# Optimization experiments

Measured on AMD Instinct MI355X. Metric: run time of the kernel, lower is better.

Reference implementation:

```python
import jax, jax.numpy as jnp
import numpy as np

N_NODES = 100000
K = 10
ALPHA = 0.1


def _gcn_norm(ei, n):
    # add self loops (PyG APPNP default: add_self_loops=True, gcn_norm)
    loops = jnp.arange(n, dtype=ei.dtype)
    src = jnp.concatenate([ei[0], loops])
    dst = jnp.concatenate([ei[1], loops])
    ones = jnp.ones(src.shape[0], dtype=jnp.float32)
    deg = jax.ops.segment_sum(ones, dst, num_segments=n)
    dinv = jnp.where(deg > 0, jax.lax.rsqrt(deg), 0.0)
    norm = dinv[src] * dinv[dst]  # [E+N]
    return src, dst, norm


def reference(x, ei, W1, b1, W2, b2):
    n = x.shape[0]
    # MLP encoder (dropout is identity in eval mode)
    h = jax.nn.relu(x @ W1 + b1)
    h = h @ W2 + b2  # [N, out_c]
    src, dst, norm = _gcn_norm(ei, n)
    h0 = h
    for _ in range(K):
        msg = norm[:, None] * h[src]                      # gather [E+N, out_c]
        agg = jax.ops.segment_sum(msg, dst, num_segments=n)  # scatter-add
        h = (1.0 - ALPHA) * agg + ALPHA * h0
    return h


def setup_inputs() -> dict:
    key = jax.random.key(0)
    k1, k2, k3, k4 = jax.random.split(key, 4)
    in_c, hidden, out_c = 512, 256, 64
    E = 3200000
    x = jax.random.normal(k1, (N_NODES, in_c), dtype=jnp.float32)
    ei = jax.random.randint(k2, (2, E), 0, N_NODES, dtype=jnp.int64)
    s1 = 1.0 / np.sqrt(in_c)
    s2 = 1.0 / np.sqrt(hidden)
    W1 = jax.random.uniform(k3, (in_c, hidden), jnp.float32, -s1, s1)
    b1 = jnp.zeros((hidden,), jnp.float32)
    W2 = jax.random.uniform(k4, (hidden, out_c), jnp.float32, -s2, s2)
    b2 = jnp.zeros((out_c,), jnp.float32)
    return {"x": x, "ei": ei, "W1": W1, "b1": b1, "W2": W2, "b2": b2}
```

## Files before the change

kernel.cpp:

```cpp
#include <hip/hip_runtime.h>


typedef unsigned short u16;
typedef unsigned int   u32;
typedef __bf16    bfx8  __attribute__((ext_vector_type(8)));
typedef _Float16  h16x8 __attribute__((ext_vector_type(8)));
typedef float     f32x4 __attribute__((ext_vector_type(4)));

#define CAP 4096
#define EPB 16384
#define NBMAX 1792

__device__ __forceinline__ u16 f2bf(float f) {
    u32 u = __float_as_uint(f);
    u += 0x7fffu + ((u >> 16) & 1u);
    return (u16)(u >> 16);
}


__global__ __launch_bounds__(256) void binscat_kernel(
        const int* __restrict__ src, const int* __restrict__ dst,
        int* __restrict__ gcur, u32* __restrict__ binned, int E, int NB) {
    __shared__ int cnt[NBMAX];
    int tid = threadIdx.x;
#pragma unroll
    for (int j = 0; j < NBMAX / 256; ++j) cnt[tid + j * 256] = 0;
    __syncthreads();
    int e0 = blockIdx.x * EPB;
    for (int r = 0; r < EPB / 256; ++r) {
        int i = e0 + r * 256 + tid;
        if (i < E) atomicAdd(&cnt[dst[i] >> 6], 1);
    }
    __syncthreads();
    for (int j = 0; j < NBMAX / 256; ++j) {
        int b = tid + j * 256;
        if (b < NB) {
            int c = cnt[b];
            cnt[b] = (c > 0) ? atomicAdd(&gcur[b], c) : 0;
        }
    }
    __syncthreads();
    for (int r = 0; r < EPB / 256; ++r) {
        int i = e0 + r * 256 + tid;
        if (i < E) {
            int d = dst[i];
            int s = src[i];
            int bb = d >> 6;
            int p = atomicAdd(&cnt[bb], 1);
            if (p < CAP) binned[(size_t)bb * CAP + p] = ((u32)(d & 63) << 17) | (u32)s;
        }
    }
}


__global__ __launch_bounds__(256) void bucket_scan_kernel(
        const int* __restrict__ gcur, int* __restrict__ bbase,
        int* __restrict__ rp, int N, int NB) {
    __shared__ int tsum[256];
    int tid = threadIdx.x;
    int loc[7];
    int run = 0;
#pragma unroll
    for (int j = 0; j < 7; ++j) {
        int b = tid * 7 + j;
        int v = 0;
        if (b < NB) { v = gcur[b]; if (v > CAP) v = CAP; }
        loc[j] = run;
        run += v;
    }
    tsum[tid] = run;
    __syncthreads();
    for (int off = 1; off < 256; off <<= 1) {
        int t = (tid >= off) ? tsum[tid - off] : 0;
        __syncthreads();
        tsum[tid] += t;
        __syncthreads();
    }
    int texcl = tsum[tid] - run;
#pragma unroll
    for (int j = 0; j < 7; ++j) {
        int b = tid * 7 + j;
        if (b < NB) bbase[b] = texcl + loc[j];
    }
    if (tid == 255) rp[N] = tsum[255];
}


__global__ __launch_bounds__(256) void buildcsr_kernel(
        const u32* __restrict__ binned, const int* __restrict__ gcur,
        const int* __restrict__ bbase, int* __restrict__ rp,
        float* __restrict__ dinv, int* __restrict__ csr, int N) {
    __shared__ u32 eb[CAP];
    __shared__ int lcsr[CAP];
    __shared__ int ncnt[64];
    __shared__ int lcur[64];
    int b = blockIdx.x;
    int tid = threadIdx.x;
    int cnt = gcur[b]; if (cnt > CAP) cnt = CAP;
    int base = bbase[b];
    if (tid < 64) ncnt[tid] = 0;
    __syncthreads();
    for (int idx = tid; idx < cnt; idx += 256) {
        u32 v = binned[(size_t)b * CAP + idx];
        eb[idx] = v;
        atomicAdd(&ncnt[v >> 17], 1);
    }
    __syncthreads();
    if (tid < 64) {
        int c = ncnt[tid];
        int s = c;
#pragma unroll
        for (int off = 1; off < 64; off <<= 1) {
            int t = __shfl_up(s, off);
            if (tid >= off) s += t;
        }
        int excl = s - c;
        lcur[tid] = excl;
        int node = b * 64 + tid;
        if (node < N) {
            rp[node] = base + excl;
            dinv[node] = rsqrtf(1.0f + (float)c);
        }
    }
    __syncthreads();
    for (int idx = tid; idx < cnt; idx += 256) {
        u32 v = eb[idx];
        int p = atomicAdd(&lcur[v >> 17], 1);
        lcsr[p] = (int)(v & 0x1FFFFu);
    }
    __syncthreads();
    for (int idx = tid; idx < cnt; idx += 256)
        csr[base + idx] = lcsr[idx];
}


__global__ void prepw1_kernel(const float* __restrict__ W1, u16* __restrict__ W1t) {
    int id = blockIdx.x * 256 + threadIdx.x;
    int k = id >> 8, n = id & 255;
    W1t[n * 512 + k] = f2bf(W1[id]);
}

__global__ void prepw2_kernel(const float* __restrict__ W2, u16* __restrict__ W2t) {
    int id = blockIdx.x * 256 + threadIdx.x;
    int k = id >> 6, n = id & 63;
    W2t[n * 256 + k] = f2bf(W2[id]);
}


__global__ __launch_bounds__(256) void mlp_kernel(
        const float* __restrict__ x, const u16* __restrict__ W1t,
        const float* __restrict__ b1, const u16* __restrict__ W2t,
        const float* __restrict__ b2, const float* __restrict__ dinv,
        float* __restrict__ h0, _Float16* __restrict__ hA, int N) {
    __shared__ char lds[65536];
    u16* xs  = (u16*)lds;
    u16* w1s = (u16*)(lds + 5120);
    u16* h1s = (u16*)lds;
    u16* w2s = (u16*)(lds + 32768);

    const int tid  = threadIdx.x;
    const int wave = tid >> 6;
    const int lane = tid & 63;
    const int lq   = lane >> 4;
    const int lr   = lane & 15;
    const int blockRow = blockIdx.x * 64;

    f32x4 acc[4][4];
#pragma unroll
    for (int a = 0; a < 4; ++a)
#pragma unroll
        for (int b = 0; b < 4; ++b) acc[a][b] = (f32x4){0.f, 0.f, 0.f, 0.f};

    for (int kk = 0; kk < 512; kk += 32) {
        __syncthreads();
        {
            int r = tid >> 2, c = (tid & 3) << 3;
            int gr = blockRow + r;
            float v[8];
            if (gr < N) {
                const float* p = x + (size_t)gr * 512 + kk + c;
                float4 u0 = *(const float4*)p;
                float4 u1 = *(const float4*)(p + 4);
                v[0]=u0.x; v[1]=u0.y; v[2]=u0.z; v[3]=u0.w;
                v[4]=u1.x; v[5]=u1.y; v[6]=u1.z; v[7]=u1.w;
            } else {
#pragma unroll
                for (int j = 0; j < 8; ++j) v[j] = 0.f;
            }
            u32 pk[4];
#pragma unroll
            for (int j = 0; j < 4; ++j)
                pk[j] = (u32)f2bf(v[2*j]) | ((u32)f2bf(v[2*j+1]) << 16);
            uint4 st = make_uint4(pk[0], pk[1], pk[2], pk[3]);
            *(uint4*)&xs[r * 40 + c] = st;
        }
        {
            const uint4* p = (const uint4*)(W1t + (size_t)tid * 512 + kk);
            uint4* q = (uint4*)&w1s[tid * 40];
            q[0] = p[0]; q[1] = p[1]; q[2] = p[2]; q[3] = p[3];
        }
        __syncthreads();
        bfx8 fa[4], fb[4];
#pragma unroll
        for (int mt = 0; mt < 4; ++mt)
            fa[mt] = *(bfx8*)&xs[(mt * 16 + lr) * 40 + lq * 8];
#pragma unroll
        for (int nt = 0; nt < 4; ++nt)
            fb[nt] = *(bfx8*)&w1s[(wave * 64 + nt * 16 + lr) * 40 + lq * 8];
#pragma unroll
        for (int mt = 0; mt < 4; ++mt)
#pragma unroll
            for (int nt = 0; nt < 4; ++nt)
                acc[mt][nt] = __builtin_amdgcn_mfma_f32_16x16x32_bf16(
                    fa[mt], fb[nt], acc[mt][nt], 0, 0, 0);
    }
    __syncthreads();

#pragma unroll
    for (int nt = 0; nt < 4; ++nt) {
        int col = wave * 64 + nt * 16 + lr;
        float bb = b1[col];
#pragma unroll
        for (int mt = 0; mt < 4; ++mt)
#pragma unroll
            for (int r = 0; r < 4; ++r) {
                int row = mt * 16 + lq * 4 + r;
                float v = acc[mt][nt][r] + bb;
                v = v > 0.f ? v : 0.f;
                h1s[row * 256 + col] = f2bf(v);
            }
    }
    {
        int nn = tid >> 2, seg = (tid & 3) * 64;
        const uint4* p = (const uint4*)(W2t + nn * 256 + seg);
        uint4* q = (uint4*)&w2s[nn * 256 + seg];
#pragma unroll
        for (int j = 0; j < 8; ++j) q[j] = p[j];
    }
    __syncthreads();

    f32x4 acc2[4];
#pragma unroll
    for (int a = 0; a < 4; ++a) acc2[a] = (f32x4){0.f, 0.f, 0.f, 0.f};
    for (int kk = 0; kk < 256; kk += 32) {
        bfx8 a = *(bfx8*)&h1s[(wave * 16 + lr) * 256 + kk + lq * 8];
#pragma unroll
        for (int nt = 0; nt < 4; ++nt) {
            bfx8 b = *(bfx8*)&w2s[(nt * 16 + lr) * 256 + kk + lq * 8];
            acc2[nt] = __builtin_amdgcn_mfma_f32_16x16x32_bf16(a, b, acc2[nt], 0, 0, 0);
        }
    }
#pragma unroll
    for (int nt = 0; nt < 4; ++nt) {
        int col = nt * 16 + lr;
        float bb = b2[col];
#pragma unroll
        for (int r = 0; r < 4; ++r) {
            int row = wave * 16 + lq * 4 + r;
            int gr = blockRow + row;
            if (gr < N) {
                float v = acc2[nt][r] + bb;
                size_t idx = (size_t)gr * 64 + col;
                h0[idx] = v;
                hA[idx] = (_Float16)(v * dinv[gr]);
            }
        }
    }
}


template <typename OUTT>
__global__ __launch_bounds__(256) void prop_kernel(
        const _Float16* __restrict__ hs, const float* __restrict__ h0,
        const float* __restrict__ dinv, const int* __restrict__ rp,
        const int* __restrict__ csr, OUTT* __restrict__ hout, int N) {
    int t = blockIdx.x * 256 + threadIdx.x;
    int i = t >> 3;
    int l = t & 7;
    if (i >= N) return;
    int beg = rp[i], end = rp[i + 1];
    const _Float16* hb = hs + l * 8;
    h16x8 self = *(const h16x8*)(hb + (size_t)i * 64);
    float a[8];
#pragma unroll
    for (int j = 0; j < 8; ++j) a[j] = (float)self[j];
    int e = beg;
    for (; e + 1 < end; e += 2) {
        int s0 = csr[e], s1 = csr[e + 1];
        h16x8 g0 = *(const h16x8*)(hb + (size_t)s0 * 64);
        h16x8 g1 = *(const h16x8*)(hb + (size_t)s1 * 64);
#pragma unroll
        for (int j = 0; j < 8; ++j) a[j] += (float)g0[j];
#pragma unroll
        for (int j = 0; j < 8; ++j) a[j] += (float)g1[j];
    }
    if (e < end) {
        int s0 = csr[e];
        h16x8 g0 = *(const h16x8*)(hb + (size_t)s0 * 64);
#pragma unroll
        for (int j = 0; j < 8; ++j) a[j] += (float)g0[j];
    }
    float dv = dinv[i];
    float c1 = 0.9f * dv;
    const float* h0p = h0 + (size_t)i * 64 + l * 8;
    float o[8];
#pragma unroll
    for (int j = 0; j < 8; ++j) o[j] = fmaf(c1, a[j], 0.1f * h0p[j]);
    if constexpr (sizeof(OUTT) == 2) {
        h16x8 ov;
#pragma unroll
        for (int j = 0; j < 8; ++j) ov[j] = (_Float16)(dv * o[j]);
        *(h16x8*)(hout + (size_t)i * 64 + l * 8) = ov;
    } else {
        float4* q = (float4*)(hout + (size_t)i * 64 + l * 8);
        q[0] = make_float4(o[0], o[1], o[2], o[3]);
        q[1] = make_float4(o[4], o[5], o[6], o[7]);
    }
}


extern "C" void kernel_launch(void* const* d_in, const int* in_sizes, int n_in,
                              void* d_out, int out_size, void* d_ws, size_t ws_size,
                              hipStream_t stream) {
    const float* x  = (const float*)d_in[0];
    const int*   ei = (const int*)d_in[1];
    const float* W1 = (const float*)d_in[2];
    const float* b1 = (const float*)d_in[3];
    const float* W2 = (const float*)d_in[4];
    const float* b2 = (const float*)d_in[5];
    const int N = in_sizes[0] / 512;
    const int E = in_sizes[1] / 2;
    const int NB = (N + 63) / 64;
    const int* src = ei;
    const int* dst = ei + E;

    char* w = (char*)d_ws;
    size_t off = 0;
    auto alloc = [&](size_t bytes) -> char* {
        char* p = w + off;
        off = (off + bytes + 1023) & ~(size_t)1023;
        return p;
    };
    int*      gcur  = (int*)alloc((size_t)NB * 4);
    int*      bbase = (int*)alloc((size_t)NB * 4);
    int*      rp    = (int*)alloc(((size_t)N + 1) * 4);
    float*    dinv  = (float*)alloc((size_t)N * 4);
    int*      csr   = (int*)alloc((size_t)E * 4);
    u32*      binned= (u32*)alloc((size_t)NB * CAP * 4);
    u16*      W1t   = (u16*)alloc(512 * 256 * 2);
    u16*      W2t   = (u16*)alloc(256 * 64 * 2);
    float*    h0    = (float*)alloc((size_t)N * 64 * 4);
    _Float16* hA    = (_Float16*)alloc((size_t)N * 64 * 2);
    _Float16* hB    = (_Float16*)alloc((size_t)N * 64 * 2);

    hipMemsetAsync(gcur, 0, (size_t)NB * 4, stream);
    binscat_kernel<<<(E + EPB - 1) / EPB, 256, 0, stream>>>(src, dst, gcur, binned, E, NB);
    bucket_scan_kernel<<<1, 256, 0, stream>>>(gcur, bbase, rp, N, NB);
    buildcsr_kernel<<<NB, 256, 0, stream>>>(binned, gcur, bbase, rp, dinv, csr, N);
    prepw1_kernel<<<512, 256, 0, stream>>>(W1, W1t);
    prepw2_kernel<<<64, 256, 0, stream>>>(W2, W2t);
    mlp_kernel<<<(N + 63) / 64, 256, 0, stream>>>(x, W1t, b1, W2t, b2, dinv, h0, hA, N);

    const _Float16* pin = hA;
    int grid = (N * 8 + 255) / 256;
    for (int it = 0; it < 9; ++it) {
        _Float16* pout = (it & 1) ? hA : hB;
        prop_kernel<_Float16><<<grid, 256, 0, stream>>>(pin, h0, dinv, rp, csr, pout, N);
        pin = pout;
    }
    prop_kernel<float><<<grid, 256, 0, stream>>>(pin, h0, dinv, rp, csr, (float*)d_out, N);
}
```

Measured before the change: 1.087 ms.

## Pre-pack MLP weights into MFMA fragment order and double-buffer x tiles

Result: faster. 1.056 ms (-2.8%).

```diff
diff --git a/kernel.cpp b/kernel.cpp
--- a/kernel.cpp
+++ b/kernel.cpp
@@ -134,29 +134,50 @@
 }
 
 
-__global__ void prepw1_kernel(const float* __restrict__ W1, u16* __restrict__ W1t) {
-    int id = blockIdx.x * 256 + threadIdx.x;
-    int k = id >> 8, n = id & 255;
-    W1t[n * 512 + k] = f2bf(W1[id]);
-}
-
-__global__ void prepw2_kernel(const float* __restrict__ W2, u16* __restrict__ W2t) {
-    int id = blockIdx.x * 256 + threadIdx.x;
-    int k = id >> 6, n = id & 63;
-    W2t[n * 256 + k] = f2bf(W2[id]);
+__global__ void prepw1_kernel(const float* __restrict__ W1, u16* __restrict__ W1f) {
+    int f = blockIdx.x * 256 + threadIdx.x;
+    int lane = f & 63;
+    int nt = (f >> 6) & 3;
+    int w  = (f >> 8) & 3;
+    int t  = f >> 10;
+    int col = w * 64 + nt * 16 + (lane & 15);
+    int k0  = t * 32 + ((lane >> 4) << 3);
+    u32 pk[4];
+#pragma unroll
+    for (int j = 0; j < 4; ++j) {
+        u16 lo = f2bf(W1[(size_t)(k0 + 2 * j) * 256 + col]);
+        u16 hi = f2bf(W1[(size_t)(k0 + 2 * j + 1) * 256 + col]);
+        pk[j] = (u32)lo | ((u32)hi << 16);
+    }
+    *(uint4*)&W1f[(size_t)f * 8] = make_uint4(pk[0], pk[1], pk[2], pk[3]);
+}
+
+__global__ void prepw2_kernel(const float* __restrict__ W2, u16* __restrict__ W2f) {
+    int f = blockIdx.x * 256 + threadIdx.x;
+    int lane = f & 63;
+    int nt = (f >> 6) & 3;
+    int t  = f >> 8;
+    int col = nt * 16 + (lane & 15);
+    int k0  = t * 32 + ((lane >> 4) << 3);
+    u32 pk[4];
+#pragma unroll
+    for (int j = 0; j < 4; ++j) {
+        u16 lo = f2bf(W2[(size_t)(k0 + 2 * j) * 64 + col]);
+        u16 hi = f2bf(W2[(size_t)(k0 + 2 * j + 1) * 64 + col]);
+        pk[j] = (u32)lo | ((u32)hi << 16);
+    }
+    *(uint4*)&W2f[(size_t)f * 8] = make_uint4(pk[0], pk[1], pk[2], pk[3]);
 }
 
 
 __global__ __launch_bounds__(256) void mlp_kernel(
-        const float* __restrict__ x, const u16* __restrict__ W1t,
-        const float* __restrict__ b1, const u16* __restrict__ W2t,
+        const float* __restrict__ x, const u16* __restrict__ W1f,
+        const float* __restrict__ b1, const u16* __restrict__ W2f,
         const float* __restrict__ b2, const float* __restrict__ dinv,
         float* __restrict__ h0, _Float16* __restrict__ hA, int N) {
-    __shared__ char lds[65536];
+    __shared__ char lds[32768];
     u16* xs  = (u16*)lds;
-    u16* w1s = (u16*)(lds + 5120);
     u16* h1s = (u16*)lds;
-    u16* w2s = (u16*)(lds + 32768);
 
     const int tid  = threadIdx.x;
     const int wave = tid >> 6;
@@ -165,54 +186,73 @@
     const int lr   = lane & 15;
     const int blockRow = blockIdx.x * 64;
 
+    const int sr = tid >> 2;
+    const int sc = (tid & 3) << 3;
+    const int gr = blockRow + sr;
+    const bool haveRow = (gr < N);
+    const float* xp = x + (size_t)(haveRow ? gr : 0) * 512 + sc;
+
     f32x4 acc[4][4];
 #pragma unroll
     for (int a = 0; a < 4; ++a)
 #pragma unroll
         for (int b = 0; b < 4; ++b) acc[a][b] = (f32x4){0.f, 0.f, 0.f, 0.f};
 
-    for (int kk = 0; kk < 512; kk += 32) {
+    {
+        float v[8];
+#pragma unroll
+        for (int j = 0; j < 8; ++j) v[j] = 0.f;
+        if (haveRow) {
+            float4 u0 = *(const float4*)(xp);
+            float4 u1 = *(const float4*)(xp + 4);
+            v[0]=u0.x; v[1]=u0.y; v[2]=u0.z; v[3]=u0.w;
+            v[4]=u1.x; v[5]=u1.y; v[6]=u1.z; v[7]=u1.w;
+        }
+        u32 pk[4];
+#pragma unroll
+        for (int j = 0; j < 4; ++j)
+            pk[j] = (u32)f2bf(v[2*j]) | ((u32)f2bf(v[2*j+1]) << 16);
+        *(uint4*)&xs[sr * 40 + sc] = make_uint4(pk[0], pk[1], pk[2], pk[3]);
+    }
+
+    const bfx8* w1q = (const bfx8*)W1f;
+
+    for (int t = 0; t < 16; ++t) {
+        bfx8 fb0 = w1q[(t * 16 + wave * 4 + 0) * 64 + lane];
+        bfx8 fb1 = w1q[(t * 16 + wave * 4 + 1) * 64 + lane];
+        bfx8 fb2 = w1q[(t * 16 + wave * 4 + 2) * 64 + lane];
+        bfx8 fb3 = w1q[(t * 16 + wave * 4 + 3) * 64 + lane];
+        float v[8];
+#pragma unroll
+        for (int j = 0; j < 8; ++j) v[j] = 0.f;
+        if (t < 15 && haveRow) {
+            const float* p = xp + (t + 1) * 32;
+            float4 u0 = *(const float4*)(p);
+            float4 u1 = *(const float4*)(p + 4);
+            v[0]=u0.x; v[1]=u0.y; v[2]=u0.z; v[3]=u0.w;
+            v[4]=u1.x; v[5]=u1.y; v[6]=u1.z; v[7]=u1.w;
+        }
         __syncthreads();
-        {
-            int r = tid >> 2, c = (tid & 3) << 3;
-            int gr = blockRow + r;
-            float v[8];
-            if (gr < N) {
-                const float* p = x + (size_t)gr * 512 + kk + c;
-                float4 u0 = *(const float4*)p;
-                float4 u1 = *(const float4*)(p + 4);
-                v[0]=u0.x; v[1]=u0.y; v[2]=u0.z; v[3]=u0.w;
-                v[4]=u1.x; v[5]=u1.y; v[6]=u1.z; v[7]=u1.w;
-            } else {
-#pragma unroll
-                for (int j = 0; j < 8; ++j) v[j] = 0.f;
-            }
+        const u16* cur = xs + (t & 1) * 2560;
+        bfx8 fa[4];
+#pragma unroll
+        for (int mt = 0; mt < 4; ++mt)
+            fa[mt] = *(const bfx8*)&cur[(mt * 16 + lr) * 40 + lq * 8];
+#pragma unroll
+        for (int mt = 0; mt < 4; ++mt) {
+            acc[mt][0] = __builtin_amdgcn_mfma_f32_16x16x32_bf16(fa[mt], fb0, acc[mt][0], 0, 0, 0);
+            acc[mt][1] = __builtin_amdgcn_mfma_f32_16x16x32_bf16(fa[mt], fb1, acc[mt][1], 0, 0, 0);
+            acc[mt][2] = __builtin_amdgcn_mfma_f32_16x16x32_bf16(fa[mt], fb2, acc[mt][2], 0, 0, 0);
+            acc[mt][3] = __builtin_amdgcn_mfma_f32_16x16x32_bf16(fa[mt], fb3, acc[mt][3], 0, 0, 0);
+        }
+        if (t < 15) {
+            u16* nxt = xs + ((t + 1) & 1) * 2560;
             u32 pk[4];
 #pragma unroll
             for (int j = 0; j < 4; ++j)
                 pk[j] = (u32)f2bf(v[2*j]) | ((u32)f2bf(v[2*j+1]) << 16);
-            uint4 st = make_uint4(pk[0], pk[1], pk[2], pk[3]);
-            *(uint4*)&xs[r * 40 + c] = st;
-        }
-        {
-            const uint4* p = (const uint4*)(W1t + (size_t)tid * 512 + kk);
-            uint4* q = (uint4*)&w1s[tid * 40];
-            q[0] = p[0]; q[1] = p[1]; q[2] = p[2]; q[3] = p[3];
-        }
-        __syncthreads();
-        bfx8 fa[4], fb[4];
-#pragma unroll
-        for (int mt = 0; mt < 4; ++mt)
-            fa[mt] = *(bfx8*)&xs[(mt * 16 + lr) * 40 + lq * 8];
-#pragma unroll
-        for (int nt = 0; nt < 4; ++nt)
-            fb[nt] = *(bfx8*)&w1s[(wave * 64 + nt * 16 + lr) * 40 + lq * 8];
-#pragma unroll
-        for (int mt = 0; mt < 4; ++mt)
-#pragma unroll
-            for (int nt = 0; nt < 4; ++nt)
-                acc[mt][nt] = __builtin_amdgcn_mfma_f32_16x16x32_bf16(
-                    fa[mt], fb[nt], acc[mt][nt], 0, 0, 0);
+            *(uint4*)&nxt[sr * 40 + sc] = make_uint4(pk[0], pk[1], pk[2], pk[3]);
+        }
     }
     __syncthreads();
 
@@ -225,31 +265,29 @@
 #pragma unroll
             for (int r = 0; r < 4; ++r) {
                 int row = mt * 16 + lq * 4 + r;
-                float v = acc[mt][nt][r] + bb;
-                v = v > 0.f ? v : 0.f;
-                h1s[row * 256 + col] = f2bf(v);
+                float vv = acc[mt][nt][r] + bb;
+                vv = vv > 0.f ? vv : 0.f;
+                h1s[row * 256 + (col ^ ((row & 7) << 3))] = f2bf(vv);
             }
     }
-    {
-        int nn = tid >> 2, seg = (tid & 3) * 64;
-        const uint4* p = (const uint4*)(W2t + nn * 256 + seg);
-        uint4* q = (uint4*)&w2s[nn * 256 + seg];
-#pragma unroll
-        for (int j = 0; j < 8; ++j) q[j] = p[j];
-    }
     __syncthreads();
 
     f32x4 acc2[4];
 #pragma unroll
     for (int a = 0; a < 4; ++a) acc2[a] = (f32x4){0.f, 0.f, 0.f, 0.f};
-    for (int kk = 0; kk < 256; kk += 32) {
-        bfx8 a = *(bfx8*)&h1s[(wave * 16 + lr) * 256 + kk + lq * 8];
+    const bfx8* w2q = (const bfx8*)W2f;
+    const int row2 = wave * 16 + lr;
+    const int sw2  = (row2 & 7) << 3;
+#pragma unroll
+    for (int t2 = 0; t2 < 8; ++t2) {
+        bfx8 a = *(const bfx8*)&h1s[row2 * 256 + ((t2 * 32 + lq * 8) ^ sw2)];
 #pragma unroll
         for (int nt = 0; nt < 4; ++nt) {
-            bfx8 b = *(bfx8*)&w2s[(nt * 16 + lr) * 256 + kk + lq * 8];
+            bfx8 b = w2q[(t2 * 4 + nt) * 64 + lane];
             acc2[nt] = __builtin_amdgcn_mfma_f32_16x16x32_bf16(a, b, acc2[nt], 0, 0, 0);
         }
     }
+
 #pragma unroll
     for (int nt = 0; nt < 4; ++nt) {
         int col = nt * 16 + lr;
@@ -257,12 +295,12 @@
 #pragma unroll
         for (int r = 0; r < 4; ++r) {
             int row = wave * 16 + lq * 4 + r;
-            int gr = blockRow + row;
-            if (gr < N) {
-                float v = acc2[nt][r] + bb;
-                size_t idx = (size_t)gr * 64 + col;
-                h0[idx] = v;
-                hA[idx] = (_Float16)(v * dinv[gr]);
+            int g = blockRow + row;
+            if (g < N) {
+                float vv = acc2[nt][r] + bb;
+                size_t idx = (size_t)g * 64 + col;
+                h0[idx] = vv;
+                hA[idx] = (_Float16)(vv * dinv[g]);
             }
         }
     }
@@ -347,8 +385,8 @@
     float*    dinv  = (float*)alloc((size_t)N * 4);
     int*      csr   = (int*)alloc((size_t)E * 4);
     u32*      binned= (u32*)alloc((size_t)NB * CAP * 4);
-    u16*      W1t   = (u16*)alloc(512 * 256 * 2);
-    u16*      W2t   = (u16*)alloc(256 * 64 * 2);
+    u16*      W1f   = (u16*)alloc(512 * 256 * 2);
+    u16*      W2f   = (u16*)alloc(256 * 64 * 2);
     float*    h0    = (float*)alloc((size_t)N * 64 * 4);
     _Float16* hA    = (_Float16*)alloc((size_t)N * 64 * 2);
     _Float16* hB    = (_Float16*)alloc((size_t)N * 64 * 2);
@@ -357,9 +395,9 @@
     binscat_kernel<<<(E + EPB - 1) / EPB, 256, 0, stream>>>(src, dst, gcur, binned, E, NB);
     bucket_scan_kernel<<<1, 256, 0, stream>>>(gcur, bbase, rp, N, NB);
     buildcsr_kernel<<<NB, 256, 0, stream>>>(binned, gcur, bbase, rp, dinv, csr, N);
-    prepw1_kernel<<<512, 256, 0, stream>>>(W1, W1t);
-    prepw2_kernel<<<64, 256, 0, stream>>>(W2, W2t);
-    mlp_kernel<<<(N + 63) / 64, 256, 0, stream>>>(x, W1t, b1, W2t, b2, dinv, h0, hA, N);
+    prepw1_kernel<<<64, 256, 0, stream>>>(W1, W1f);
+    prepw2_kernel<<<8, 256, 0, stream>>>(W2, W2f);
+    mlp_kernel<<<(N + 63) / 64, 256, 0, stream>>>(x, W1f, b1, W2f, b2, dinv, h0, hA, N);
 
     const _Float16* pin = hA;
     int grid = (N * 8 + 255) / 256;
```
